# Kernel optimization log

Measured on AMD Instinct MI355X. Metric: run time of the kernel, lower is better.

## Reference

```python
import jax, jax.numpy as jnp
import numpy as np

D = 64   # input_dim = number of tiny MLPs
H = 64   # hidden_dim
L = 2    # num_hidden_layers
B = 32768


def setup_inputs() -> dict:
    key = jax.random.key(0)
    ks = jax.random.split(key, 14)
    s = 0.1
    return {
        "x": jax.random.normal(ks[0], (B, 2 * D), dtype=jnp.float32),
        # bank of D tiny MLPs, params stacked along leading expert dim
        "h_w1": jax.random.normal(ks[1], (D, H), dtype=jnp.float32) * s,   # Linear(1,H) weight per expert
        "h_b1": jax.random.normal(ks[2], (D, H), dtype=jnp.float32) * s,
        "h_wh": jax.random.normal(ks[3], (L, D, H, H), dtype=jnp.float32) * s,
        "h_bh": jax.random.normal(ks[4], (L, D, H), dtype=jnp.float32) * s,
        "h_wo": jax.random.normal(ks[5], (D, H), dtype=jnp.float32) * s,   # Linear(H,1) weight per expert
        "h_bo": jax.random.normal(ks[6], (D,), dtype=jnp.float32) * s,
        # larger model_g MLP
        "g_w1": jax.random.normal(ks[7], (D, H), dtype=jnp.float32) * s,
        "g_b1": jax.random.normal(ks[8], (H,), dtype=jnp.float32) * s,
        "g_wh": jax.random.normal(ks[9], (L, H, H), dtype=jnp.float32) * s,
        "g_bh": jax.random.normal(ks[10], (L, H), dtype=jnp.float32) * s,
        "g_wo": jax.random.normal(ks[11], (H,), dtype=jnp.float32) * s,
        "g_bo": jax.random.normal(ks[12], (1,), dtype=jnp.float32) * s,
    }


def reference(x, h_w1, h_b1, h_wh, h_bh, h_wo, h_bo,
              g_w1, g_b1, g_wh, g_bh, g_wo, g_bo):
    first = x[:, :D]    # [B, D] -> model_g input
    second = x[:, D:]   # [B, D] -> one scalar column per tiny MLP

    # --- bank of D tiny MLPs, fused as batched GEMMs over expert dim d ---
    # input layer: Linear(1,H): h[b,d,:] = relu(second[b,d] * w1[d,:] + b1[d,:])
    h = jax.nn.relu(second[:, :, None] * h_w1[None, :, :] + h_b1[None, :, :])  # [B,D,H]
    for l in range(L):
        h = jax.nn.relu(jnp.einsum('bdh,dhk->bdk', h, h_wh[l]) + h_bh[l][None, :, :])
    h_out = jnp.einsum('bdh,dh->bd', h, h_wo) + h_bo[None, :]  # [B, D]

    # --- model_g: standard MLP on first half ---
    g = jax.nn.relu(first @ g_w1 + g_b1)          # [B, H]
    for l in range(L):
        g = jax.nn.relu(g @ g_wh[l] + g_bh[l])
    g_out = g @ g_wo[:, None] + g_bo              # [B, 1]

    return h_out, g_out
```

## Files before the change

kernel.cpp:

```cpp
#include <hip/hip_runtime.h>

typedef __attribute__((ext_vector_type(4))) float  f32x4;
typedef __attribute__((ext_vector_type(8))) __bf16 bf16x8;

__device__ __forceinline__ int Pq(int q) {
  return ((q >> 5) << 5) + (((q >> 2) & 3) << 3) + (((q >> 4) & 1) << 2) + (q & 3);
}
__device__ __forceinline__ float cut16(float v) {
  return __uint_as_float(__float_as_uint(v) & 0xFFFF0000u);
}

#define HSZ 11264

__global__ void reformat_w(const float* __restrict__ h_w1, const float* __restrict__ h_b1,
                           const float* __restrict__ h_wh, const float* __restrict__ h_wo,
                           const float* __restrict__ g_w1, const float* __restrict__ g_wh,
                           __bf16* __restrict__ wsH, __bf16* __restrict__ wsG)
{
  int i = blockIdx.x * 256 + threadIdx.x;
  if (i < 64 * HSZ) {
    int d = i / HSZ, o = i - d * HSZ;
    int e = o & 511, j = e & 7, lane = e >> 3, c = lane & 15, g4 = lane >> 4;
    float val = 0.f;
    if (o < 2048) {
      int mf = o >> 9;
      if (g4 == 0 && j <= 4) {
        int Pc = Pq((mf << 4) | c);
        float w1 = h_w1[(d << 6) + Pc], b1 = h_b1[(d << 6) + Pc];
        float w1h = cut16(w1), b1h = cut16(b1);
        val = (j == 1) ? b1h : (j == 3) ? (w1 - w1h) : (j == 4) ? (b1 - b1h) : w1h;
      }
    } else if (o < 10240) {
      int o2 = o - 2048;
      int l = o2 >> 12, f = (o2 >> 9) & 7;
      int mf = f >> 1, kk = f & 1;
      int krow = (kk << 5) + (g4 << 3) + j;
      int mcol = Pq((mf << 4) | c);
      val = h_wh[(((l << 6) + d) << 12) + (krow << 6) + mcol];
    } else {
      int o3 = o - 10240;
      int kk = o3 >> 9;
      int k = (kk << 5) + (g4 << 3) + j;
      float wo = h_wo[(d << 6) + k];
      float woh = cut16(wo);
      val = (c == 0) ? woh : (c == 1) ? (wo - woh) : 0.f;
    }
    wsH[i] = (__bf16)val;
  } else if (i < 64 * HSZ + 12288) {
    int t = i - 64 * HSZ;
    int j = t & 7, lane = (t >> 3) & 63, f = (t >> 9) & 7;
    int c = lane & 15, g4 = lane >> 4, mf = f >> 1, kk = f & 1;
    int krow = (kk << 5) + (g4 << 3) + j;
    int mcol = Pq((mf << 4) + c);
    int lg = t >> 12;
    const float* W = (lg == 0) ? g_w1 : g_wh + ((lg - 1) << 12);
    wsG[t] = (__bf16)W[(krow << 6) + mcol];
  }
}

__device__ __forceinline__ void rebuild(const f32x4 (&acc)[4][4], bf16x8 (&bfr)[4][2]) {
  #pragma unroll
  for (int nf = 0; nf < 4; ++nf)
    #pragma unroll
    for (int kk = 0; kk < 2; ++kk) {
      bf16x8 v;
      #pragma unroll
      for (int e = 0; e < 8; ++e)
        v[e] = (__bf16)fmaxf(acc[(kk << 1) | (e >> 2)][nf][e & 3], 0.f);
      bfr[nf][kk] = v;
    }
}

__device__ __forceinline__ void layer(const __bf16* __restrict__ wf,
                                      const float* __restrict__ bias,
                                      int lane, int g4, bool do_rebuild,
                                      f32x4 (&acc)[4][4], bf16x8 (&bfr)[4][2])
{
  bf16x8 aw0[4], aw1[4];
  #pragma unroll
  for (int mf = 0; mf < 4; ++mf) {
    aw0[mf] = *(const bf16x8*)&wf[((mf << 1) << 9) + (lane << 3)];
    aw1[mf] = *(const bf16x8*)&wf[(((mf << 1) | 1) << 9) + (lane << 3)];
  }
  f32x4 bv[4];
  #pragma unroll
  for (int mf = 0; mf < 4; ++mf)
    bv[mf] = *(const f32x4*)&bias[((mf >> 1) << 5) + (g4 << 3) + ((mf & 1) << 2)];
  #pragma unroll
  for (int mf = 0; mf < 4; ++mf)
    #pragma unroll
    for (int nf = 0; nf < 4; ++nf)
      acc[mf][nf] = __builtin_amdgcn_mfma_f32_16x16x32_bf16(aw0[mf], bfr[nf][0], bv[mf], 0, 0, 0);
  #pragma unroll
  for (int mf = 0; mf < 4; ++mf)
    #pragma unroll
    for (int nf = 0; nf < 4; ++nf)
      acc[mf][nf] = __builtin_amdgcn_mfma_f32_16x16x32_bf16(aw1[mf], bfr[nf][1], acc[mf][nf], 0, 0, 0);
  if (do_rebuild) rebuild(acc, bfr);
}

__global__ __launch_bounds__(512, 4) void fused_nn(
    const float* __restrict__ x,
    const float* __restrict__ h_bh, const float* __restrict__ h_bo,
    const float* __restrict__ g_b1, const float* __restrict__ g_bh,
    const float* __restrict__ g_wo, const float* __restrict__ g_bo,
    const __bf16* __restrict__ wsH, const __bf16* __restrict__ wsG,
    float* __restrict__ out, int Btot, int nwg)
{
  __shared__ float sOut[64 * 33];

  const int tid  = threadIdx.x;
  const int lane = tid & 63;
  const int wid  = tid >> 6;
  const int c    = lane & 15;
  const int g4   = lane >> 4;

  const int b0  = blockIdx.x;
  const int bid = (b0 & 7) * (nwg >> 3) + (b0 >> 3);
  const int unit = bid / 17;
  const int s    = bid - unit * 17;

  f32x4  acc[4][4];
  bf16x8 bfr[4][2];
  const f32x4 z = {0.f, 0.f, 0.f, 0.f};

  if (s < 16) {
    const int nb = (unit << 9) + ((s >> 1) << 6);
    const int d0 = (s & 1) << 5;

    #pragma unroll 1
    for (int dl = 0; dl < 4; ++dl) {
      const int d = d0 + (wid << 2) + dl;
      const __bf16* base = wsH + d * HSZ;

      #pragma unroll
      for (int nf = 0; nf < 4; ++nf) {
        float sv = 0.f;
        if (g4 == 0) sv = x[(size_t)(nb + (nf << 4) + c) * 128 + 64 + d];
        float shf = cut16(sv);
        __bf16 sh = (__bf16)shf, sl = (__bf16)(sv - shf);
        bf16x8 v = {};
        v[0] = sh; v[1] = (__bf16)1.0f; v[2] = sl; v[3] = sh; v[4] = (__bf16)1.0f;
        bfr[nf][0] = v;
      }

      {
        bf16x8 a1[4];
        #pragma unroll
        for (int mf = 0; mf < 4; ++mf)
          a1[mf] = *(const bf16x8*)&base[(mf << 9) + (lane << 3)];
        #pragma unroll
        for (int mf = 0; mf < 4; ++mf)
          #pragma unroll
          for (int nf = 0; nf < 4; ++nf)
            acc[mf][nf] = __builtin_amdgcn_mfma_f32_16x16x32_bf16(a1[mf], bfr[nf][0], z, 0, 0, 0);
        rebuild(acc, bfr);
      }

      layer(base + 2048, h_bh + (d << 6),        lane, g4, true, acc, bfr);
      layer(base + 6144, h_bh + ((64 + d) << 6), lane, g4, true, acc, bfr);

      {
        bf16x8 wo0 = *(const bf16x8*)&base[10240 + (lane << 3)];
        bf16x8 wo1 = *(const bf16x8*)&base[10240 + 512 + (lane << 3)];
        float bo = h_bo[d];
        #pragma unroll
        for (int nf = 0; nf < 4; ++nf) {
          f32x4 e2 = __builtin_amdgcn_mfma_f32_16x16x32_bf16(wo0, bfr[nf][0], z, 0, 0, 0);
          e2 = __builtin_amdgcn_mfma_f32_16x16x32_bf16(wo1, bfr[nf][1], e2, 0, 0, 0);
          if (g4 == 0)
            sOut[((nf << 4) + c) * 33 + (wid << 2) + dl] = e2[0] + e2[1] + bo;
        }
      }
    }

    __syncthreads();
    {
      const int r = tid >> 3, q = tid & 7;
      const float* sp = &sOut[r * 33 + (q << 2)];
      f32x4 v = { sp[0], sp[1], sp[2], sp[3] };
      *(f32x4*)&out[(size_t)(nb + r) * 64 + d0 + (q << 2)] = v;
    }

  } else {
    const int nb = (unit << 9) + (wid << 6);

    #pragma unroll
    for (int nf = 0; nf < 4; ++nf) {
      const float* xr = x + (size_t)(nb + (nf << 4) + c) * 128;
      #pragma unroll
      for (int kk = 0; kk < 2; ++kk) {
        f32x4 v0 = *(const f32x4*)&xr[(kk << 5) + (g4 << 3)];
        f32x4 v1 = *(const f32x4*)&xr[(kk << 5) + (g4 << 3) + 4];
        bf16x8 v;
        #pragma unroll
        for (int r = 0; r < 4; ++r) { v[r] = (__bf16)v0[r]; v[4 + r] = (__bf16)v1[r]; }
        bfr[nf][kk] = v;
      }
    }
    layer(wsG,        g_b1,      lane, g4, true,  acc, bfr);
    layer(wsG + 4096, g_bh,      lane, g4, true,  acc, bfr);
    layer(wsG + 8192, g_bh + 64, lane, g4, false, acc, bfr);

    f32x4 wv[4];
    #pragma unroll
    for (int mf = 0; mf < 4; ++mf)
      wv[mf] = *(const f32x4*)&g_wo[((mf >> 1) << 5) + (g4 << 3) + ((mf & 1) << 2)];
    float p[4] = {0.f, 0.f, 0.f, 0.f};
    #pragma unroll
    for (int mf = 0; mf < 4; ++mf)
      #pragma unroll
      for (int nf = 0; nf < 4; ++nf)
        #pragma unroll
        for (int r = 0; r < 4; ++r)
          p[nf] += fmaxf(acc[mf][nf][r], 0.f) * wv[mf][r];
    #pragma unroll
    for (int nf = 0; nf < 4; ++nf) {
      p[nf] += __shfl_xor(p[nf], 16);
      p[nf] += __shfl_xor(p[nf], 32);
    }
    float sel = (g4 == 0) ? p[0] : (g4 == 1) ? p[1] : (g4 == 2) ? p[2] : p[3];
    out[((size_t)Btot << 6) + nb + lane] = sel + g_bo[0];
  }
}

extern "C" void kernel_launch(void* const* d_in, const int* in_sizes, int n_in,
                              void* d_out, int out_size, void* d_ws, size_t ws_size,
                              hipStream_t stream) {
  const float* x    = (const float*)d_in[0];
  const float* h_w1 = (const float*)d_in[1];
  const float* h_b1 = (const float*)d_in[2];
  const float* h_wh = (const float*)d_in[3];
  const float* h_bh = (const float*)d_in[4];
  const float* h_wo = (const float*)d_in[5];
  const float* h_bo = (const float*)d_in[6];
  const float* g_w1 = (const float*)d_in[7];
  const float* g_b1 = (const float*)d_in[8];
  const float* g_wh = (const float*)d_in[9];
  const float* g_bh = (const float*)d_in[10];
  const float* g_wo = (const float*)d_in[11];
  const float* g_bo = (const float*)d_in[12];

  __bf16* wsH = (__bf16*)d_ws;
  __bf16* wsG = wsH + 64 * HSZ;

  const int Btot  = in_sizes[0] / 128;
  const int nUnit = Btot >> 9;
  const int nwg   = nUnit * 17;

  hipLaunchKernelGGL(reformat_w, dim3(2864), dim3(256), 0, stream,
                     h_w1, h_b1, h_wh, h_wo, g_w1, g_wh, wsH, wsG);

  hipLaunchKernelGGL(fused_nn, dim3(nwg), dim3(512), 0, stream,
                     x, h_bh, h_bo,
                     g_b1, g_bh, g_wo, g_bo,
                     (const __bf16*)wsH, (const __bf16*)wsG,
                     (float*)d_out, Btot, nwg);
}
```

Measured before the change: 83.39 us.

## Stage per-expert weights in LDS with double-buffered async global-to-LDS loads

Restructures the expert-bank work split so each 256-thread block handles 16 experts for 256 rows. Each expert's reformatted weights are loaded once into shared memory through async global_load_lds, double-buffered, and shared by all four waves. Previously every wave read its own expert's weights straight from global memory. This cuts redundant global and L2 weight traffic and overlaps the next expert's load with the current compute. In exchange it adds a block-wide barrier per expert, uses about 45KB of LDS per block, and changes the grid shape and launch bounds.

```diff
diff --git a/kernel.cpp b/kernel.cpp
--- a/kernel.cpp
+++ b/kernel.cpp
@@ -1,4 +1,5 @@
 #include <hip/hip_runtime.h>
+#include <stdint.h>
 
 typedef __attribute__((ext_vector_type(4))) float  f32x4;
 typedef __attribute__((ext_vector_type(8))) __bf16 bf16x8;
@@ -11,6 +12,10 @@
 }
 
 #define HSZ 11264
+
+#define GL2LDS(gp, lp) __builtin_amdgcn_global_load_lds(                     \
+    (const __attribute__((address_space(1))) uint32_t*)(gp),                 \
+    (__attribute__((address_space(3))) uint32_t*)(lp), 16, 0, 0)
 
 __global__ void reformat_w(const float* __restrict__ h_w1, const float* __restrict__ h_b1,
                            const float* __restrict__ h_wh, const float* __restrict__ h_wo,
@@ -99,7 +104,17 @@
   if (do_rebuild) rebuild(acc, bfr);
 }
 
-__global__ __launch_bounds__(512, 4) void fused_nn(
+__device__ __forceinline__ void stageW(const __bf16* __restrict__ src, __bf16* dst,
+                                       int wid, int lane) {
+  #pragma unroll
+  for (int u = 0; u < 6; ++u) {
+    int ch = (u << 2) + wid;
+    if (ch < 22)
+      GL2LDS(src + (ch << 9) + (lane << 3), dst + (ch << 9));
+  }
+}
+
+__global__ __launch_bounds__(256, 2) void fused_nn(
     const float* __restrict__ x,
     const float* __restrict__ h_bh, const float* __restrict__ h_bo,
     const float* __restrict__ g_b1, const float* __restrict__ g_bh,
@@ -107,7 +122,8 @@
     const __bf16* __restrict__ wsH, const __bf16* __restrict__ wsG,
     float* __restrict__ out, int Btot, int nwg)
 {
-  __shared__ float sOut[64 * 33];
+  __shared__ __bf16 sW[2][HSZ];
+  __shared__ float  sOut[256 * 17];
 
   const int tid  = threadIdx.x;
   const int lane = tid & 63;
@@ -117,74 +133,90 @@
 
   const int b0  = blockIdx.x;
   const int bid = (b0 & 7) * (nwg >> 3) + (b0 >> 3);
-  const int unit = bid / 17;
-  const int s    = bid - unit * 17;
-
-  f32x4  acc[4][4];
-  bf16x8 bfr[4][2];
+  const int unit = bid / 5;
+  const int s    = bid - unit * 5;
+
   const f32x4 z = {0.f, 0.f, 0.f, 0.f};
 
-  if (s < 16) {
-    const int nb = (unit << 9) + ((s >> 1) << 6);
-    const int d0 = (s & 1) << 5;
+  if (s < 4) {
+    const int d0  = s << 4;
+    const int nbw = (unit << 8) + (wid << 6);
+
+    stageW(wsH + d0 * HSZ, sW[0], wid, lane);
+    __syncthreads();
 
     #pragma unroll 1
-    for (int dl = 0; dl < 4; ++dl) {
-      const int d = d0 + (wid << 2) + dl;
-      const __bf16* base = wsH + d * HSZ;
-
-      #pragma unroll
-      for (int nf = 0; nf < 4; ++nf) {
-        float sv = 0.f;
-        if (g4 == 0) sv = x[(size_t)(nb + (nf << 4) + c) * 128 + 64 + d];
-        float shf = cut16(sv);
-        __bf16 sh = (__bf16)shf, sl = (__bf16)(sv - shf);
-        bf16x8 v = {};
-        v[0] = sh; v[1] = (__bf16)1.0f; v[2] = sl; v[3] = sh; v[4] = (__bf16)1.0f;
-        bfr[nf][0] = v;
-      }
-
-      {
-        bf16x8 a1[4];
-        #pragma unroll
-        for (int mf = 0; mf < 4; ++mf)
-          a1[mf] = *(const bf16x8*)&base[(mf << 9) + (lane << 3)];
-        #pragma unroll
-        for (int mf = 0; mf < 4; ++mf)
-          #pragma unroll
-          for (int nf = 0; nf < 4; ++nf)
-            acc[mf][nf] = __builtin_amdgcn_mfma_f32_16x16x32_bf16(a1[mf], bfr[nf][0], z, 0, 0, 0);
-        rebuild(acc, bfr);
-      }
-
-      layer(base + 2048, h_bh + (d << 6),        lane, g4, true, acc, bfr);
-      layer(base + 6144, h_bh + ((64 + d) << 6), lane, g4, true, acc, bfr);
-
-      {
-        bf16x8 wo0 = *(const bf16x8*)&base[10240 + (lane << 3)];
-        bf16x8 wo1 = *(const bf16x8*)&base[10240 + 512 + (lane << 3)];
-        float bo = h_bo[d];
+    for (int tg = 0; tg < 4; ++tg) {
+      f32x4 xq[4];
+      #pragma unroll
+      for (int nf = 0; nf < 4; ++nf)
+        xq[nf] = *(const f32x4*)&x[(size_t)(nbw + (nf << 4) + c) * 128 + 64 + d0 + (tg << 2)];
+
+      #pragma unroll
+      for (int ti = 0; ti < 4; ++ti) {
+        const int t = (tg << 2) + ti;
+        const int d = d0 + t;
+        const __bf16* Wb = sW[ti & 1];
+
+        if (t < 15) stageW(wsH + (d + 1) * HSZ, sW[1 - (ti & 1)], wid, lane);
+
+        bf16x8 b0[4];
         #pragma unroll
         for (int nf = 0; nf < 4; ++nf) {
-          f32x4 e2 = __builtin_amdgcn_mfma_f32_16x16x32_bf16(wo0, bfr[nf][0], z, 0, 0, 0);
-          e2 = __builtin_amdgcn_mfma_f32_16x16x32_bf16(wo1, bfr[nf][1], e2, 0, 0, 0);
-          if (g4 == 0)
-            sOut[((nf << 4) + c) * 33 + (wid << 2) + dl] = e2[0] + e2[1] + bo;
+          float sv  = xq[nf][ti];
+          float shf = cut16(sv);
+          bf16x8 v = {};
+          v[0] = (__bf16)shf; v[1] = (__bf16)1.0f; v[2] = (__bf16)(sv - shf);
+          v[3] = (__bf16)shf; v[4] = (__bf16)1.0f;
+          b0[nf] = v;
         }
+
+        f32x4  acc[4][4];
+        bf16x8 bfr[4][2];
+        {
+          bf16x8 a1[4];
+          #pragma unroll
+          for (int mf = 0; mf < 4; ++mf)
+            a1[mf] = *(const bf16x8*)&Wb[(mf << 9) + (lane << 3)];
+          #pragma unroll
+          for (int mf = 0; mf < 4; ++mf)
+            #pragma unroll
+            for (int nf = 0; nf < 4; ++nf)
+              acc[mf][nf] = __builtin_amdgcn_mfma_f32_16x16x32_bf16(a1[mf], b0[nf], z, 0, 0, 0);
+          rebuild(acc, bfr);
+        }
+        layer(Wb + 2048, h_bh + (d << 6),        lane, g4, true, acc, bfr);
+        layer(Wb + 6144, h_bh + ((64 + d) << 6), lane, g4, true, acc, bfr);
+
+        {
+          bf16x8 wo0 = *(const bf16x8*)&Wb[10240 + (lane << 3)];
+          bf16x8 wo1 = *(const bf16x8*)&Wb[10752 + (lane << 3)];
+          float bo = h_bo[d];
+          #pragma unroll
+          for (int nf = 0; nf < 4; ++nf) {
+            f32x4 e2 = __builtin_amdgcn_mfma_f32_16x16x32_bf16(wo0, bfr[nf][0], z, 0, 0, 0);
+            e2 = __builtin_amdgcn_mfma_f32_16x16x32_bf16(wo1, bfr[nf][1], e2, 0, 0, 0);
+            if (g4 == 0)
+              sOut[((wid << 6) + (nf << 4) + c) * 17 + t] = e2[0] + e2[1] + bo;
+          }
+        }
+        __syncthreads();
       }
     }
 
-    __syncthreads();
-    {
-      const int r = tid >> 3, q = tid & 7;
-      const float* sp = &sOut[r * 33 + (q << 2)];
+    #pragma unroll
+    for (int i = 0; i < 4; ++i) {
+      int r = (i << 6) + (tid >> 2), q = tid & 3;
+      const float* sp = &sOut[r * 17 + (q << 2)];
       f32x4 v = { sp[0], sp[1], sp[2], sp[3] };
-      *(f32x4*)&out[(size_t)(nb + r) * 64 + d0 + (q << 2)] = v;
+      *(f32x4*)&out[(size_t)((unit << 8) + r) * 64 + d0 + (q << 2)] = v;
     }
 
   } else {
-    const int nb = (unit << 9) + (wid << 6);
-
+    const int nb = (unit << 8) + (wid << 6);
+
+    f32x4  acc[4][4];
+    bf16x8 bfr[4][2];
     #pragma unroll
     for (int nf = 0; nf < 4; ++nf) {
       const float* xr = x + (size_t)(nb + (nf << 4) + c) * 128;
@@ -245,13 +277,13 @@
   __bf16* wsG = wsH + 64 * HSZ;
 
   const int Btot  = in_sizes[0] / 128;
-  const int nUnit = Btot >> 9;
-  const int nwg   = nUnit * 17;
+  const int nUnit = Btot >> 8;
+  const int nwg   = nUnit * 5;
 
   hipLaunchKernelGGL(reformat_w, dim3(2864), dim3(256), 0, stream,
                      h_w1, h_b1, h_wh, h_wo, g_w1, g_wh, wsH, wsG);
 
-  hipLaunchKernelGGL(fused_nn, dim3(nwg), dim3(512), 0, stream,
+  hipLaunchKernelGGL(fused_nn, dim3(nwg), dim3(256), 0, stream,
                      x, h_bh, h_bo,
                      g_b1, g_bh, g_wo, g_bo,
                      (const __bf16*)wsH, (const __bf16*)wsG,
```

Measured after the change: 70.12 us. -15.9%, faster.
